# Performance work log

Hardware: AMD Instinct MI355X
Metric: run time of the kernel (lower is better)

The kernel has to match this reference:

```python
import jax, jax.numpy as jnp
import numpy as np

WS = 8      # window_size
SS = 4      # shift_size
DIM = 64
B, H, W = 4, 256, 256
EPS = 1e-12


def _conv(x, w, groups=1, pad=0):
    return jax.lax.conv_general_dilated(
        x, w, window_strides=(1, 1), padding=[(pad, pad), (pad, pad)],
        feature_group_count=groups,
        dimension_numbers=('NCHW', 'OIHW', 'NCHW'))


def _window_partition(x, ws):
    # Faithful to torch: permute (B,C,nh,ws,nw,ws)->(B,C,nh,nw,ws,ws) then flat view(-1,C,ws,ws)
    b, c, h, w = x.shape
    pb, pr = (-h) % ws, (-w) % ws
    if pb or pr:
        x = jnp.pad(x, ((0, 0), (0, 0), (0, pb), (0, pr)))
    h2, w2 = h + pb, w + pr
    x = x.reshape(b, c, h2 // ws, ws, w2 // ws, ws).transpose(0, 1, 2, 4, 3, 5)
    return x.reshape(-1, c, ws, ws)


def _window_reverse(win, ws, h, w):
    pb, pr = (-h) % ws, (-w) % ws
    h2, w2 = h + pb, w + pr
    b = win.shape[0] * ws * ws // (h2 * w2)
    x = win.reshape(b, -1, h2 // ws, w2 // ws, ws, ws).transpose(0, 1, 2, 4, 3, 5)
    x = x.reshape(b, -1, h2, w2)
    return x[:, :, :h, :w]


def _chan_attn(q, k, v, temp):
    # channel (transposed) attention on flattened window pixels
    n, c = q.shape[0], q.shape[1]
    q = q.reshape(n, c, -1)
    k = k.reshape(n, c, -1)
    v = v.reshape(n, c, -1)
    q = q / jnp.maximum(jnp.linalg.norm(q, axis=-1, keepdims=True), EPS)
    k = k / jnp.maximum(jnp.linalg.norm(k, axis=-1, keepdims=True), EPS)
    attn = jax.nn.softmax(jnp.einsum('ncd,nkd->nck', q, k) / temp, axis=-1)
    out = jnp.einsum('nck,nkd->ncd', attn, v)
    return out.reshape(n, c, WS, WS)


def setup_inputs() -> dict:
    key = jax.random.key(0)
    ks = jax.random.split(key, 10)
    C = DIM
    p = lambda k, s: jax.random.normal(k, s, jnp.float32) * 0.05
    return {
        'x': jax.random.normal(ks[0], (B, C, H, W), jnp.float32),
        'x_f': jax.random.normal(ks[1], (B, C, H, W), jnp.float32),
        'temperature': jnp.ones((1,), jnp.float32),
        'qk_w': p(ks[2], (2 * C, C, 1, 1)),
        'qk_dw_w': p(ks[3], (2 * C, 1, 3, 3)),
        'v_w': p(ks[4], (C, C, 1, 1)),
        'v_dw_w': p(ks[5], (C, 1, 3, 3)),
        'proj_w': p(ks[6], (C, C, 3, 3)),
        'proj1_w': p(ks[7], (C, C, 3, 3)),
        'qkv1_w': p(ks[8], (3 * C, C, 1, 1)),
        'qkv1_dw_w': p(ks[9], (3 * C, 1, 3, 3)),
    }


def reference(x, x_f, temperature, qk_w, qk_dw_w, v_w, v_dw_w,
              proj_w, proj1_w, qkv1_w, qkv1_dw_w):
    b, c, h, w = x.shape
    xw = _window_partition(x, WS)
    xfw = _window_partition(x_f, WS)

    qk = _conv(_conv(xfw, qk_w), qk_dw_w, groups=2 * c, pad=1)
    v = _conv(_conv(xw, v_w), v_dw_w, groups=c, pad=1)
    q, k = jnp.split(qk, 2, axis=1)
    out = _chan_attn(q, k, v, temperature)
    out = _conv(out, proj_w, pad=1)
    out = _window_reverse(out, WS, h, w)

    shift = jnp.roll(out, (-SS, -SS), axis=(2, 3))
    sw = _window_partition(shift, WS)
    qkv = _conv(_conv(sw, qkv1_w), qkv1_dw_w, groups=3 * c, pad=1)
    q, k, v = jnp.split(qkv, 3, axis=1)
    out = _chan_attn(q, k, v, temperature)
    out = _conv(out, proj1_w, pad=1)
    out = _window_reverse(out, WS, h, w)
    out = jnp.roll(out, (SS, SS), axis=(2, 3))
    return out
```

## Files before the change

### kernel.cpp

```cpp
#include <hip/hip_runtime.h>

typedef short v8s __attribute__((ext_vector_type(8)));
typedef _Float16 v8h __attribute__((ext_vector_type(8)));
typedef float v4f __attribute__((ext_vector_type(4)));
typedef unsigned short u16;

#define MFMA_F16(a, b, c) __builtin_amdgcn_mfma_f32_16x16x32_f16((a), (b), (c), 0, 0, 0)
#define XS 72

__device__ __forceinline__ u16 f16r(float x) {
    _Float16 h = (_Float16)x; u16 u; __builtin_memcpy(&u, &h, 2); return u;
}
__device__ __forceinline__ float f16f(u16 u) {
    _Float16 h; __builtin_memcpy(&h, &u, 2); return (float)h;
}

__device__ __forceinline__ void mm_frags(const u16* __restrict__ Ag,
                                         const u16* __restrict__ XB,
                                         int wv, int L, int q, v4f C[4])
{
#pragma unroll
    for (int nt = 0; nt < 4; ++nt) C[nt] = (v4f){0.f, 0.f, 0.f, 0.f};
#pragma unroll
    for (int kt = 0; kt < 2; ++kt) {
        v8h a = *(const v8h*)(Ag + (16 * wv + L) * 64 + kt * 32 + q * 8);
#pragma unroll
        for (int nt = 0; nt < 4; ++nt) {
            v8h b = *(const v8h*)(XB + (nt * 16 + L) * XS + kt * 32 + q * 8);
            C[nt] = MFMA_F16(a, b, C[nt]);
        }
    }
}
__device__ __forceinline__ void mm_store(const v4f C[4], u16* __restrict__ M,
                                         int wv, int L, int q)
{
    const int rowb = 16 * wv + 4 * q;
#pragma unroll
    for (int r = 0; r < 4; ++r)
#pragma unroll
        for (int nt = 0; nt < 4; ++nt)
            M[(rowb + r) * XS + nt * 16 + L] = f16r(C[nt][r]);
}
__device__ __forceinline__ void mm_stage(const u16* __restrict__ Ag,
                                         const u16* __restrict__ XB,
                                         u16* __restrict__ M,
                                         int wv, int L, int q)
{
    v4f C[4];
    mm_frags(Ag, XB, wv, L, q, C);
    mm_store(C, M, wv, L, q);
}

__device__ __forceinline__ void dw_read(const u16* __restrict__ M, int c, int r0,
                                        v8s raw[4])
{
#pragma unroll
    for (int r = 0; r < 4; ++r) {
        const int rr = r0 - 1 + r;
        raw[r] = ((unsigned)rr < 8u) ? *(const v8s*)(M + c * XS + rr * 8)
                                     : (v8s){0, 0, 0, 0, 0, 0, 0, 0};
    }
}

template <bool TR, bool NORM>
__device__ __forceinline__ void dw_write(const float* __restrict__ dwg,
                                         const v8s raw[4], int c, int r0,
                                         u16* __restrict__ Out)
{
    float w[9];
#pragma unroll
    for (int k = 0; k < 9; ++k) w[k] = dwg[c * 9 + k];
    float in[4][10];
#pragma unroll
    for (int r = 0; r < 4; ++r) {
        in[r][0] = 0.f; in[r][9] = 0.f;
#pragma unroll
        for (int j = 0; j < 8; ++j) in[r][j + 1] = f16f((u16)raw[r][j]);
    }
    float o[2][8];
#pragma unroll
    for (int rr = 0; rr < 2; ++rr)
#pragma unroll
        for (int j = 0; j < 8; ++j) {
            float s;
            s = w[0] * in[rr][j];
            s = fmaf(w[1], in[rr][j + 1], s);
            s = fmaf(w[2], in[rr][j + 2], s);
            s = fmaf(w[3], in[rr + 1][j], s);
            s = fmaf(w[4], in[rr + 1][j + 1], s);
            s = fmaf(w[5], in[rr + 1][j + 2], s);
            s = fmaf(w[6], in[rr + 2][j], s);
            s = fmaf(w[7], in[rr + 2][j + 1], s);
            s = fmaf(w[8], in[rr + 2][j + 2], s);
            o[rr][j] = s;
        }
    if (NORM) {
        float ss = 0.f;
#pragma unroll
        for (int rr = 0; rr < 2; ++rr)
#pragma unroll
            for (int j = 0; j < 8; ++j) ss = fmaf(o[rr][j], o[rr][j], ss);
        ss += __shfl_xor(ss, 1);
        ss += __shfl_xor(ss, 2);
        const float sc = 1.0f / fmaxf(sqrtf(ss), 1e-12f);
#pragma unroll
        for (int rr = 0; rr < 2; ++rr)
#pragma unroll
            for (int j = 0; j < 8; ++j) o[rr][j] *= sc;
    }
    if (TR) {
#pragma unroll
        for (int rr = 0; rr < 2; ++rr)
#pragma unroll
            for (int j = 0; j < 8; ++j)
                Out[((r0 + rr) * 8 + j) * XS + c] = f16r(o[rr][j]);
    } else {
#pragma unroll
        for (int rr = 0; rr < 2; ++rr) {
            v8s v;
#pragma unroll
            for (int j = 0; j < 8; ++j) v[j] = (short)f16r(o[rr][j]);
            *(v8s*)(Out + c * XS + (r0 + rr) * 8) = v;
        }
    }
}

__device__ __forceinline__ void mm_lds(const u16* __restrict__ Am,
                                       const u16* __restrict__ Bm,
                                       int wv, int L, int q, v4f C[4])
{
#pragma unroll
    for (int nt = 0; nt < 4; ++nt) C[nt] = (v4f){0.f, 0.f, 0.f, 0.f};
#pragma unroll
    for (int kt = 0; kt < 2; ++kt) {
        v8h a = *(const v8h*)(Am + (16 * wv + L) * XS + kt * 32 + q * 8);
#pragma unroll
        for (int nt = 0; nt < 4; ++nt) {
            v8h b = *(const v8h*)(Bm + (nt * 16 + L) * XS + kt * 32 + q * 8);
            C[nt] = MFMA_F16(a, b, C[nt]);
        }
    }
}

__device__ __forceinline__ void proj_mm(const u16* __restrict__ Wg,
                                        const u16* __restrict__ Ot,
                                        int wv, int L, int q, v4f C[4])
{
#pragma unroll
    for (int nt = 0; nt < 4; ++nt) C[nt] = (v4f){0.f, 0.f, 0.f, 0.f};
    const u16* arow = Wg + (16 * wv + L) * 576;
    const int pc = L & 7;
    const int prb = L >> 3;
#pragma unroll
    for (int tap = 0; tap < 9; ++tap) {
        const int dy = tap / 3 - 1, dx = tap % 3 - 1;
        const int spc = pc + dx;
        const bool vc = (unsigned)spc < 8u;
#pragma unroll
        for (int half = 0; half < 2; ++half) {
            v8h a = *(const v8h*)(arow + tap * 64 + half * 32 + q * 8);
#pragma unroll
            for (int nt = 0; nt < 4; ++nt) {
                const int spr = nt * 2 + prb + dy;
                v8h b = (v8h)0;
                if (vc && (unsigned)spr < 8u)
                    b = *(const v8h*)(Ot + (spr * 8 + spc) * XS + half * 32 + q * 8);
                C[nt] = MFMA_F16(a, b, C[nt]);
            }
        }
    }
}

__device__ __forceinline__ void softmax_to_lds(v4f S[4], float invt,
                                               u16* __restrict__ Am,
                                               int rowb, int L)
{
#pragma unroll
    for (int nt = 0; nt < 4; ++nt) S[nt] *= invt;
#pragma unroll
    for (int r = 0; r < 4; ++r) {
        float mx = fmaxf(fmaxf(S[0][r], S[1][r]), fmaxf(S[2][r], S[3][r]));
        mx = fmaxf(mx, __shfl_xor(mx, 1));
        mx = fmaxf(mx, __shfl_xor(mx, 2));
        mx = fmaxf(mx, __shfl_xor(mx, 4));
        mx = fmaxf(mx, __shfl_xor(mx, 8));
        float e0 = __expf(S[0][r] - mx);
        float e1 = __expf(S[1][r] - mx);
        float e2 = __expf(S[2][r] - mx);
        float e3 = __expf(S[3][r] - mx);
        float sm = e0 + e1 + e2 + e3;
        sm += __shfl_xor(sm, 1);
        sm += __shfl_xor(sm, 2);
        sm += __shfl_xor(sm, 4);
        sm += __shfl_xor(sm, 8);
        const float ri = 1.0f / sm;
        Am[(rowb + r) * XS + L +  0] = f16r(e0 * ri);
        Am[(rowb + r) * XS + L + 16] = f16r(e1 * ri);
        Am[(rowb + r) * XS + L + 32] = f16r(e2 * ri);
        Am[(rowb + r) * XS + L + 48] = f16r(e3 * ri);
    }
}

__global__ void prep(const float* __restrict__ qk_w, const float* __restrict__ v_w,
                     const float* __restrict__ qkv_w, const float* __restrict__ pw0,
                     const float* __restrict__ pw1, u16* __restrict__ Wb)
{
    int i = blockIdx.x * 256 + threadIdx.x;
    float v;
    if (i < 8192) v = qk_w[i];
    else if (i < 12288) v = v_w[i - 8192];
    else if (i < 24576) v = qkv_w[i - 12288];
    else {
        int j = i - 24576;
        const float* s = pw0;
        if (j >= 36864) { s = pw1; j -= 36864; }
        const int o = j / 576, kk = j % 576;
        const int tap = kk >> 6, c = kk & 63;
        v = s[o * 576 + c * 9 + tap];
    }
    Wb[i] = f16r(v);
}

__global__ __launch_bounds__(256, 4) void k1(
    const float* __restrict__ x, const float* __restrict__ xf,
    const float* __restrict__ temp_p,
    const float* __restrict__ qk_dw, const float* __restrict__ v_dw,
    const u16* __restrict__ Wqk, const u16* __restrict__ Wv,
    const u16* __restrict__ Wp0,
    u16* __restrict__ midb)
{
    __shared__ u16 B0[64 * XS], B1[64 * XS], B2[64 * XS], B3[64 * XS];
    const int t = threadIdx.x, n = blockIdx.x;
    const int lane = t & 63, wv = t >> 6, L = lane & 15, q = lane >> 4;
    const int rowb = 16 * wv + 4 * q;
    const size_t base = (size_t)n << 12;
    const float invt = 1.0f / temp_p[0];
    const int yp = t >> 4, xx0 = (t & 15) << 4;
    const int c2b = (yp >> 3) << 5, ir = (yp & 7) << 3;
    const int dc = t >> 2, dr0 = (t & 3) << 1;

    float4 rx[4];
    {
        const float* sf = xf + base + yp * 256 + xx0;
        const float* sx = x  + base + yp * 256 + xx0;
#pragma unroll
        for (int k = 0; k < 4; ++k) {
            float4 a = *(const float4*)(sf + 4 * k);
            rx[k] = *(const float4*)(sx + 4 * k);
            const int xx = xx0 + 4 * k;
            const int c = c2b + (xx >> 3), pb = ir + (xx & 7);
            B0[(pb + 0) * XS + c] = f16r(a.x);
            B0[(pb + 1) * XS + c] = f16r(a.y);
            B0[(pb + 2) * XS + c] = f16r(a.z);
            B0[(pb + 3) * XS + c] = f16r(a.w);
        }
    }
    __syncthreads();
    mm_stage(Wqk,        B0, B1, wv, L, q);
    mm_stage(Wqk + 4096, B0, B2, wv, L, q);
    __syncthreads();
    {
#pragma unroll
        for (int k = 0; k < 4; ++k) {
            const int xx = xx0 + 4 * k;
            const int c = c2b + (xx >> 3), pb = ir + (xx & 7);
            B3[(pb + 0) * XS + c] = f16r(rx[k].x);
            B3[(pb + 1) * XS + c] = f16r(rx[k].y);
            B3[(pb + 2) * XS + c] = f16r(rx[k].z);
            B3[(pb + 3) * XS + c] = f16r(rx[k].w);
        }
    }
    v8s rawA[4];
    dw_read(B1, dc, dr0, rawA);
    __syncthreads();
    mm_stage(Wv, B3, B0, wv, L, q);
    dw_write<false, true>(qk_dw, rawA, dc, dr0, B1);
    v8s rawB[4];
    dw_read(B2, dc, dr0, rawB);
    __syncthreads();
    dw_write<false, true>(qk_dw + 576, rawB, dc, dr0, B2);
    dw_read(B0, dc, dr0, rawA);
    dw_write<true, false>(v_dw, rawA, dc, dr0, B3);
    __syncthreads();
    v4f S[4];
    mm_lds(B1, B2, wv, L, q, S);
    softmax_to_lds(S, invt, B1, rowb, L);
    __syncthreads();
    v4f O[4];
    mm_lds(B1, B3, wv, L, q, O);
#pragma unroll
    for (int nt = 0; nt < 4; ++nt)
#pragma unroll
        for (int r = 0; r < 4; ++r)
            B2[(L + 16 * nt) * XS + rowb + r] = f16r(O[nt][r]);
    __syncthreads();
    v4f C[4];
    proj_mm(Wp0, B2, wv, L, q, C);
#pragma unroll
    for (int nt = 0; nt < 4; ++nt)
#pragma unroll
        for (int r = 0; r < 4; ++r) {
            const int o = rowb + r, p = L + 16 * nt;
            const int yy = ((o >> 5) << 3) + (p >> 3);
            const int xp = ((o & 31) << 3) + (p & 7);
            midb[base + yy * 256 + xp] = f16r(C[nt][r]);
        }
}

__global__ __launch_bounds__(256, 4) void k2(
    const u16* __restrict__ midb, const float* __restrict__ temp_p,
    const float* __restrict__ qkv_dw,
    const u16* __restrict__ Wqkv, const u16* __restrict__ Wp1,
    float* __restrict__ out)
{
    __shared__ u16 B0[64 * XS], B1[64 * XS], B2[64 * XS];
    const int t = threadIdx.x, m = blockIdx.x;
    const int lane = t & 63, wv = t >> 6, L = lane & 15, q = lane >> 4;
    const int rowb = 16 * wv + 4 * q;
    const int plane = m >> 4, mh2 = m & 15;
    const u16* img = midb + ((size_t)plane << 16);
    const float invt = 1.0f / temp_p[0];
    const int yp = t >> 4, xx0 = (t & 15) << 4;
    const int c2b = (yp >> 3) << 5, ir = (yp & 7) << 3;
    const int dc = t >> 2, dr0 = (t & 3) << 1;

    {
        const int row = (mh2 * 16 + 4 + yp) & 255;
#pragma unroll
        for (int k = 0; k < 4; ++k) {
            const int cc = (xx0 + 4 + 4 * k) & 255;
            ushort4 a = *(const ushort4*)(img + row * 256 + cc);
            const int xx = xx0 + 4 * k;
            const int c = c2b + (xx >> 3), pb = ir + (xx & 7);
            B0[(pb + 0) * XS + c] = a.x;
            B0[(pb + 1) * XS + c] = a.y;
            B0[(pb + 2) * XS + c] = a.z;
            B0[(pb + 3) * XS + c] = a.w;
        }
    }
    __syncthreads();
    mm_stage(Wqkv,        B0, B1, wv, L, q);
    mm_stage(Wqkv + 4096, B0, B2, wv, L, q);
    v4f VF[4];
    mm_frags(Wqkv + 8192, B0, wv, L, q, VF);
    __syncthreads();
    mm_store(VF, B0, wv, L, q);
    v8s rawQ[4];
    dw_read(B1, dc, dr0, rawQ);
    __syncthreads();
    dw_write<false, true>(qkv_dw, rawQ, dc, dr0, B1);
    v8s rawK[4];
    dw_read(B2, dc, dr0, rawK);
    v8s rawV[4];
    dw_read(B0, dc, dr0, rawV);
    __syncthreads();
    dw_write<false, true>(qkv_dw + 576, rawK, dc, dr0, B2);
    dw_write<true, false>(qkv_dw + 1152, rawV, dc, dr0, B0);
    __syncthreads();
    v4f S[4];
    mm_lds(B1, B2, wv, L, q, S);
    softmax_to_lds(S, invt, B1, rowb, L);
    v4f O[4];
    mm_lds(B1, B0, wv, L, q, O);
    __syncthreads();
#pragma unroll
    for (int nt = 0; nt < 4; ++nt)
#pragma unroll
        for (int r = 0; r < 4; ++r)
            B2[(L + 16 * nt) * XS + rowb + r] = f16r(O[nt][r]);
    __syncthreads();
    v4f C[4];
    proj_mm(Wp1, B2, wv, L, q, C);
    float* op = out + ((size_t)plane << 16);
#pragma unroll
    for (int nt = 0; nt < 4; ++nt)
#pragma unroll
        for (int r = 0; r < 4; ++r) {
            const int o = rowb + r, p = L + 16 * nt;
            const int R = mh2 * 16 + ((o >> 5) << 3) + (p >> 3);
            const int orow = (R + 4) & 255;
            const int ocol = ((o & 31) * 8 + (p & 7) + 4) & 255;
            op[orow * 256 + ocol] = C[nt][r];
        }
}

extern "C" void kernel_launch(void* const* d_in, const int* in_sizes, int n_in,
                              void* d_out, int out_size, void* d_ws, size_t ws_size,
                              hipStream_t stream)
{
    const float* x       = (const float*)d_in[0];
    const float* xf      = (const float*)d_in[1];
    const float* temp    = (const float*)d_in[2];
    const float* qk_w    = (const float*)d_in[3];
    const float* qk_dw   = (const float*)d_in[4];
    const float* v_w     = (const float*)d_in[5];
    const float* v_dw    = (const float*)d_in[6];
    const float* proj_w  = (const float*)d_in[7];
    const float* proj1_w = (const float*)d_in[8];
    const float* qkv1_w  = (const float*)d_in[9];
    const float* qkv1_dw = (const float*)d_in[10];
    float* out = (float*)d_out;

    u16* midb = (u16*)d_ws;
    u16* Wb   = (u16*)((char*)d_ws + 33554432);

    prep<<<384, 256, 0, stream>>>(qk_w, v_w, qkv1_w, proj_w, proj1_w, Wb);
    k1<<<4096, 256, 0, stream>>>(x, xf, temp, qk_dw, v_dw,
                                 Wb, Wb + 8192, Wb + 24576, midb);
    k2<<<4096, 256, 0, stream>>>(midb, temp, qkv1_dw,
                                 Wb + 12288, Wb + 61440, out);
}
```

Measured before the change: 291.8 us.

## Restructure k1 stage schedule to cut barriers and add MFMA wave priority

In k1, x and x_f are both converted into LDS in the initial load loop. The V projection is computed as register fragments alongside the QK projections, mirroring k2's schedule, which removes one barrier and a register-held staging of x. A barrier between softmax and the attention-V matmul is dropped. s_setprio raises wave priority around MFMA sections in both kernels so matrix work is favoured over other waves. These changes shift the buffer-role assignments, and dropping the barrier relies on each wave reading only the softmax rows it wrote.

```diff
diff --git a/kernel.cpp b/kernel.cpp
--- a/kernel.cpp
+++ b/kernel.cpp
@@ -239,55 +239,56 @@
     const int c2b = (yp >> 3) << 5, ir = (yp & 7) << 3;
     const int dc = t >> 2, dr0 = (t & 3) << 1;
 
-    float4 rx[4];
     {
         const float* sf = xf + base + yp * 256 + xx0;
         const float* sx = x  + base + yp * 256 + xx0;
 #pragma unroll
         for (int k = 0; k < 4; ++k) {
             float4 a = *(const float4*)(sf + 4 * k);
-            rx[k] = *(const float4*)(sx + 4 * k);
+            float4 b = *(const float4*)(sx + 4 * k);
             const int xx = xx0 + 4 * k;
             const int c = c2b + (xx >> 3), pb = ir + (xx & 7);
             B0[(pb + 0) * XS + c] = f16r(a.x);
             B0[(pb + 1) * XS + c] = f16r(a.y);
             B0[(pb + 2) * XS + c] = f16r(a.z);
             B0[(pb + 3) * XS + c] = f16r(a.w);
-        }
-    }
-    __syncthreads();
+            B3[(pb + 0) * XS + c] = f16r(b.x);
+            B3[(pb + 1) * XS + c] = f16r(b.y);
+            B3[(pb + 2) * XS + c] = f16r(b.z);
+            B3[(pb + 3) * XS + c] = f16r(b.w);
+        }
+    }
+    __syncthreads();
+    __builtin_amdgcn_s_setprio(1);
     mm_stage(Wqk,        B0, B1, wv, L, q);
     mm_stage(Wqk + 4096, B0, B2, wv, L, q);
-    __syncthreads();
-    {
-#pragma unroll
-        for (int k = 0; k < 4; ++k) {
-            const int xx = xx0 + 4 * k;
-            const int c = c2b + (xx >> 3), pb = ir + (xx & 7);
-            B3[(pb + 0) * XS + c] = f16r(rx[k].x);
-            B3[(pb + 1) * XS + c] = f16r(rx[k].y);
-            B3[(pb + 2) * XS + c] = f16r(rx[k].z);
-            B3[(pb + 3) * XS + c] = f16r(rx[k].w);
-        }
-    }
-    v8s rawA[4];
-    dw_read(B1, dc, dr0, rawA);
-    __syncthreads();
-    mm_stage(Wv, B3, B0, wv, L, q);
-    dw_write<false, true>(qk_dw, rawA, dc, dr0, B1);
-    v8s rawB[4];
-    dw_read(B2, dc, dr0, rawB);
-    __syncthreads();
-    dw_write<false, true>(qk_dw + 576, rawB, dc, dr0, B2);
-    dw_read(B0, dc, dr0, rawA);
-    dw_write<true, false>(v_dw, rawA, dc, dr0, B3);
+    v4f VF[4];
+    mm_frags(Wv, B3, wv, L, q, VF);
+    __builtin_amdgcn_s_setprio(0);
+    __syncthreads();
+    mm_store(VF, B3, wv, L, q);
+    v8s rawQ[4];
+    dw_read(B1, dc, dr0, rawQ);
+    __syncthreads();
+    dw_write<false, true>(qk_dw, rawQ, dc, dr0, B1);
+    v8s rawK[4];
+    dw_read(B2, dc, dr0, rawK);
+    v8s rawV[4];
+    dw_read(B3, dc, dr0, rawV);
+    __syncthreads();
+    dw_write<false, true>(qk_dw + 576, rawK, dc, dr0, B2);
+    dw_write<true, false>(v_dw, rawV, dc, dr0, B0);
     __syncthreads();
     v4f S[4];
+    __builtin_amdgcn_s_setprio(1);
     mm_lds(B1, B2, wv, L, q, S);
+    __builtin_amdgcn_s_setprio(0);
     softmax_to_lds(S, invt, B1, rowb, L);
-    __syncthreads();
     v4f O[4];
-    mm_lds(B1, B3, wv, L, q, O);
+    __builtin_amdgcn_s_setprio(1);
+    mm_lds(B1, B0, wv, L, q, O);
+    __builtin_amdgcn_s_setprio(0);
+    __syncthreads();
 #pragma unroll
     for (int nt = 0; nt < 4; ++nt)
 #pragma unroll
@@ -295,7 +296,9 @@
             B2[(L + 16 * nt) * XS + rowb + r] = f16r(O[nt][r]);
     __syncthreads();
     v4f C[4];
+    __builtin_amdgcn_s_setprio(1);
     proj_mm(Wp0, B2, wv, L, q, C);
+    __builtin_amdgcn_s_setprio(0);
 #pragma unroll
     for (int nt = 0; nt < 4; ++nt)
 #pragma unroll
@@ -339,10 +342,12 @@
         }
     }
     __syncthreads();
+    __builtin_amdgcn_s_setprio(1);
     mm_stage(Wqkv,        B0, B1, wv, L, q);
     mm_stage(Wqkv + 4096, B0, B2, wv, L, q);
     v4f VF[4];
     mm_frags(Wqkv + 8192, B0, wv, L, q, VF);
+    __builtin_amdgcn_s_setprio(0);
     __syncthreads();
     mm_store(VF, B0, wv, L, q);
     v8s rawQ[4];
@@ -358,10 +363,14 @@
     dw_write<true, false>(qkv_dw + 1152, rawV, dc, dr0, B0);
     __syncthreads();
     v4f S[4];
+    __builtin_amdgcn_s_setprio(1);
     mm_lds(B1, B2, wv, L, q, S);
+    __builtin_amdgcn_s_setprio(0);
     softmax_to_lds(S, invt, B1, rowb, L);
     v4f O[4];
+    __builtin_amdgcn_s_setprio(1);
     mm_lds(B1, B0, wv, L, q, O);
+    __builtin_amdgcn_s_setprio(0);
     __syncthreads();
 #pragma unroll
     for (int nt = 0; nt < 4; ++nt)
@@ -370,7 +379,9 @@
             B2[(L + 16 * nt) * XS + rowb + r] = f16r(O[nt][r]);
     __syncthreads();
     v4f C[4];
+    __builtin_amdgcn_s_setprio(1);
     proj_mm(Wp1, B2, wv, L, q, C);
+    __builtin_amdgcn_s_setprio(0);
     float* op = out + ((size_t)plane << 16);
 #pragma unroll
     for (int nt = 0; nt < 4; ++nt)
```

New measurement: 291.1 us. About the same (-0.2%).

## Process two window tiles per block in k1 and k2 to interleave work

Applied to the files above, without the earlier changes.

Each block in both kernels now handles two independent tiles, using doubled LDS buffers and interleaving their matmul, depthwise and softmax stages. This halves the block count and the barriers per tile, and gives the scheduler independent MFMA and LDS work to overlap. In exchange register and LDS use per block roughly doubles, and launch bounds drop to 2 blocks per SM, which lowers occupancy. k1's buffer usage is reorganised from four buffers to three per tile, with the V projection moved to register fragments.

```diff
diff --git a/kernel.cpp b/kernel.cpp
--- a/kernel.cpp
+++ b/kernel.cpp
@@ -221,7 +221,7 @@
     Wb[i] = f16r(v);
 }
 
-__global__ __launch_bounds__(256, 4) void k1(
+__global__ __launch_bounds__(256, 2) void k1(
     const float* __restrict__ x, const float* __restrict__ xf,
     const float* __restrict__ temp_p,
     const float* __restrict__ qk_dw, const float* __restrict__ v_dw,
@@ -229,73 +229,107 @@
     const u16* __restrict__ Wp0,
     u16* __restrict__ midb)
 {
-    __shared__ u16 B0[64 * XS], B1[64 * XS], B2[64 * XS], B3[64 * XS];
-    const int t = threadIdx.x, n = blockIdx.x;
+    __shared__ u16 B0a[64 * XS], B1a[64 * XS], B2a[64 * XS];
+    __shared__ u16 B0b[64 * XS], B1b[64 * XS], B2b[64 * XS];
+    const int t = threadIdx.x;
+    const int n0 = blockIdx.x << 1, n1 = n0 + 1;
     const int lane = t & 63, wv = t >> 6, L = lane & 15, q = lane >> 4;
     const int rowb = 16 * wv + 4 * q;
-    const size_t base = (size_t)n << 12;
+    const size_t base0 = (size_t)n0 << 12, base1 = (size_t)n1 << 12;
     const float invt = 1.0f / temp_p[0];
     const int yp = t >> 4, xx0 = (t & 15) << 4;
     const int c2b = (yp >> 3) << 5, ir = (yp & 7) << 3;
     const int dc = t >> 2, dr0 = (t & 3) << 1;
 
-    float4 rx[4];
+    float4 rx0[4], rx1[4];
     {
-        const float* sf = xf + base + yp * 256 + xx0;
-        const float* sx = x  + base + yp * 256 + xx0;
+        const float* sf0 = xf + base0 + yp * 256 + xx0;
+        const float* sx0 = x  + base0 + yp * 256 + xx0;
+        const float* sf1 = xf + base1 + yp * 256 + xx0;
+        const float* sx1 = x  + base1 + yp * 256 + xx0;
 #pragma unroll
         for (int k = 0; k < 4; ++k) {
-            float4 a = *(const float4*)(sf + 4 * k);
-            rx[k] = *(const float4*)(sx + 4 * k);
+            float4 a0 = *(const float4*)(sf0 + 4 * k);
+            float4 a1 = *(const float4*)(sf1 + 4 * k);
+            rx0[k] = *(const float4*)(sx0 + 4 * k);
+            rx1[k] = *(const float4*)(sx1 + 4 * k);
             const int xx = xx0 + 4 * k;
             const int c = c2b + (xx >> 3), pb = ir + (xx & 7);
-            B0[(pb + 0) * XS + c] = f16r(a.x);
-            B0[(pb + 1) * XS + c] = f16r(a.y);
-            B0[(pb + 2) * XS + c] = f16r(a.z);
-            B0[(pb + 3) * XS + c] = f16r(a.w);
-        }
-    }
-    __syncthreads();
-    mm_stage(Wqk,        B0, B1, wv, L, q);
-    mm_stage(Wqk + 4096, B0, B2, wv, L, q);
+            B0a[(pb + 0) * XS + c] = f16r(a0.x);
+            B0a[(pb + 1) * XS + c] = f16r(a0.y);
+            B0a[(pb + 2) * XS + c] = f16r(a0.z);
+            B0a[(pb + 3) * XS + c] = f16r(a0.w);
+            B0b[(pb + 0) * XS + c] = f16r(a1.x);
+            B0b[(pb + 1) * XS + c] = f16r(a1.y);
+            B0b[(pb + 2) * XS + c] = f16r(a1.z);
+            B0b[(pb + 3) * XS + c] = f16r(a1.w);
+        }
+    }
+    __syncthreads();
+    mm_stage(Wqk,        B0a, B1a, wv, L, q);
+    mm_stage(Wqk + 4096, B0a, B2a, wv, L, q);
+    mm_stage(Wqk,        B0b, B1b, wv, L, q);
+    mm_stage(Wqk + 4096, B0b, B2b, wv, L, q);
     __syncthreads();
     {
 #pragma unroll
         for (int k = 0; k < 4; ++k) {
             const int xx = xx0 + 4 * k;
             const int c = c2b + (xx >> 3), pb = ir + (xx & 7);
-            B3[(pb + 0) * XS + c] = f16r(rx[k].x);
-            B3[(pb + 1) * XS + c] = f16r(rx[k].y);
-            B3[(pb + 2) * XS + c] = f16r(rx[k].z);
-            B3[(pb + 3) * XS + c] = f16r(rx[k].w);
-        }
-    }
-    v8s rawA[4];
-    dw_read(B1, dc, dr0, rawA);
-    __syncthreads();
-    mm_stage(Wv, B3, B0, wv, L, q);
-    dw_write<false, true>(qk_dw, rawA, dc, dr0, B1);
-    v8s rawB[4];
-    dw_read(B2, dc, dr0, rawB);
-    __syncthreads();
-    dw_write<false, true>(qk_dw + 576, rawB, dc, dr0, B2);
-    dw_read(B0, dc, dr0, rawA);
-    dw_write<true, false>(v_dw, rawA, dc, dr0, B3);
-    __syncthreads();
-    v4f S[4];
-    mm_lds(B1, B2, wv, L, q, S);
-    softmax_to_lds(S, invt, B1, rowb, L);
-    __syncthreads();
-    v4f O[4];
-    mm_lds(B1, B3, wv, L, q, O);
+            B0a[(pb + 0) * XS + c] = f16r(rx0[k].x);
+            B0a[(pb + 1) * XS + c] = f16r(rx0[k].y);
+            B0a[(pb + 2) * XS + c] = f16r(rx0[k].z);
+            B0a[(pb + 3) * XS + c] = f16r(rx0[k].w);
+            B0b[(pb + 0) * XS + c] = f16r(rx1[k].x);
+            B0b[(pb + 1) * XS + c] = f16r(rx1[k].y);
+            B0b[(pb + 2) * XS + c] = f16r(rx1[k].z);
+            B0b[(pb + 3) * XS + c] = f16r(rx1[k].w);
+        }
+    }
+    v8s rawQ0[4], rawQ1[4];
+    dw_read(B1a, dc, dr0, rawQ0);
+    dw_read(B1b, dc, dr0, rawQ1);
+    __syncthreads();
+    v4f VF0[4], VF1[4];
+    mm_frags(Wv, B0a, wv, L, q, VF0);
+    mm_frags(Wv, B0b, wv, L, q, VF1);
+    dw_write<false, true>(qk_dw, rawQ0, dc, dr0, B1a);
+    dw_write<false, true>(qk_dw, rawQ1, dc, dr0, B1b);
+    v8s rawK0[4], rawK1[4];
+    dw_read(B2a, dc, dr0, rawK0);
+    dw_read(B2b, dc, dr0, rawK1);
+    __syncthreads();
+    mm_store(VF0, B0a, wv, L, q);
+    mm_store(VF1, B0b, wv, L, q);
+    dw_write<false, true>(qk_dw + 576, rawK0, dc, dr0, B2a);
+    dw_write<false, true>(qk_dw + 576, rawK1, dc, dr0, B2b);
+    __syncthreads();
+    v8s rawV0[4], rawV1[4];
+    dw_read(B0a, dc, dr0, rawV0);
+    dw_read(B0b, dc, dr0, rawV1);
+    v4f S0[4], S1[4];
+    mm_lds(B1a, B2a, wv, L, q, S0);
+    mm_lds(B1b, B2b, wv, L, q, S1);
+    softmax_to_lds(S0, invt, B1a, rowb, L);
+    softmax_to_lds(S1, invt, B1b, rowb, L);
+    __syncthreads();
+    dw_write<true, false>(v_dw, rawV0, dc, dr0, B0a);
+    dw_write<true, false>(v_dw, rawV1, dc, dr0, B0b);
+    __syncthreads();
+    v4f O0[4], O1[4];
+    mm_lds(B1a, B0a, wv, L, q, O0);
+    mm_lds(B1b, B0b, wv, L, q, O1);
 #pragma unroll
     for (int nt = 0; nt < 4; ++nt)
 #pragma unroll
-        for (int r = 0; r < 4; ++r)
-            B2[(L + 16 * nt) * XS + rowb + r] = f16r(O[nt][r]);
-    __syncthreads();
-    v4f C[4];
-    proj_mm(Wp0, B2, wv, L, q, C);
+        for (int r = 0; r < 4; ++r) {
+            B2a[(L + 16 * nt) * XS + rowb + r] = f16r(O0[nt][r]);
+            B2b[(L + 16 * nt) * XS + rowb + r] = f16r(O1[nt][r]);
+        }
+    __syncthreads();
+    v4f C0[4], C1[4];
+    proj_mm(Wp0, B2a, wv, L, q, C0);
+    proj_mm(Wp0, B2b, wv, L, q, C1);
 #pragma unroll
     for (int nt = 0; nt < 4; ++nt)
 #pragma unroll
@@ -303,84 +337,114 @@
             const int o = rowb + r, p = L + 16 * nt;
             const int yy = ((o >> 5) << 3) + (p >> 3);
             const int xp = ((o & 31) << 3) + (p & 7);
-            midb[base + yy * 256 + xp] = f16r(C[nt][r]);
-        }
-}
-
-__global__ __launch_bounds__(256, 4) void k2(
+            midb[base0 + yy * 256 + xp] = f16r(C0[nt][r]);
+            midb[base1 + yy * 256 + xp] = f16r(C1[nt][r]);
+        }
+}
+
+__global__ __launch_bounds__(256, 2) void k2(
     const u16* __restrict__ midb, const float* __restrict__ temp_p,
     const float* __restrict__ qkv_dw,
     const u16* __restrict__ Wqkv, const u16* __restrict__ Wp1,
     float* __restrict__ out)
 {
-    __shared__ u16 B0[64 * XS], B1[64 * XS], B2[64 * XS];
-    const int t = threadIdx.x, m = blockIdx.x;
+    __shared__ u16 B0a[64 * XS], B1a[64 * XS], B2a[64 * XS];
+    __shared__ u16 B0b[64 * XS], B1b[64 * XS], B2b[64 * XS];
+    const int t = threadIdx.x;
+    const int m0 = blockIdx.x << 1, m1 = m0 + 1;
     const int lane = t & 63, wv = t >> 6, L = lane & 15, q = lane >> 4;
     const int rowb = 16 * wv + 4 * q;
-    const int plane = m >> 4, mh2 = m & 15;
-    const u16* img = midb + ((size_t)plane << 16);
+    const int plane0 = m0 >> 4, mh0 = m0 & 15;
+    const int plane1 = m1 >> 4, mh1 = m1 & 15;
+    const u16* img0 = midb + ((size_t)plane0 << 16);
+    const u16* img1 = midb + ((size_t)plane1 << 16);
     const float invt = 1.0f / temp_p[0];
     const int yp = t >> 4, xx0 = (t & 15) << 4;
     const int c2b = (yp >> 3) << 5, ir = (yp & 7) << 3;
     const int dc = t >> 2, dr0 = (t & 3) << 1;
 
     {
-        const int row = (mh2 * 16 + 4 + yp) & 255;
+        const int row0 = (mh0 * 16 + 4 + yp) & 255;
+        const int row1 = (mh1 * 16 + 4 + yp) & 255;
 #pragma unroll
         for (int k = 0; k < 4; ++k) {
             const int cc = (xx0 + 4 + 4 * k) & 255;
-            ushort4 a = *(const ushort4*)(img + row * 256 + cc);
+            ushort4 a0 = *(const ushort4*)(img0 + row0 * 256 + cc);
+            ushort4 a1 = *(const ushort4*)(img1 + row1 * 256 + cc);
             const int xx = xx0 + 4 * k;
             const int c = c2b + (xx >> 3), pb = ir + (xx & 7);
-            B0[(pb + 0) * XS + c] = a.x;
-            B0[(pb + 1) * XS + c] = a.y;
-            B0[(pb + 2) * XS + c] = a.z;
-            B0[(pb + 3) * XS + c] = a.w;
-        }
-    }
-    __syncthreads();
-    mm_stage(Wqkv,        B0, B1, wv, L, q);
-    mm_stage(Wqkv + 4096, B0, B2, wv, L, q);
-    v4f VF[4];
-    mm_frags(Wqkv + 8192, B0, wv, L, q, VF);
-    __syncthreads();
-    mm_store(VF, B0, wv, L, q);
-    v8s rawQ[4];
-    dw_read(B1, dc, dr0, rawQ);
-    __syncthreads();
-    dw_write<false, true>(qkv_dw, rawQ, dc, dr0, B1);
-    v8s rawK[4];
-    dw_read(B2, dc, dr0, rawK);
-    v8s rawV[4];
-    dw_read(B0, dc, dr0, rawV);
-    __syncthreads();
-    dw_write<false, true>(qkv_dw + 576, rawK, dc, dr0, B2);
-    dw_write<true, false>(qkv_dw + 1152, rawV, dc, dr0, B0);
-    __syncthreads();
-    v4f S[4];
-    mm_lds(B1, B2, wv, L, q, S);
-    softmax_to_lds(S, invt, B1, rowb, L);
-    v4f O[4];
-    mm_lds(B1, B0, wv, L, q, O);
+            B0a[(pb + 0) * XS + c] = a0.x;
+            B0a[(pb + 1) * XS + c] = a0.y;
+            B0a[(pb + 2) * XS + c] = a0.z;
+            B0a[(pb + 3) * XS + c] = a0.w;
+            B0b[(pb + 0) * XS + c] = a1.x;
+            B0b[(pb + 1) * XS + c] = a1.y;
+            B0b[(pb + 2) * XS + c] = a1.z;
+            B0b[(pb + 3) * XS + c] = a1.w;
+        }
+    }
+    __syncthreads();
+    mm_stage(Wqkv,        B0a, B1a, wv, L, q);
+    mm_stage(Wqkv + 4096, B0a, B2a, wv, L, q);
+    v4f VF0[4], VF1[4];
+    mm_frags(Wqkv + 8192, B0a, wv, L, q, VF0);
+    mm_stage(Wqkv,        B0b, B1b, wv, L, q);
+    mm_stage(Wqkv + 4096, B0b, B2b, wv, L, q);
+    mm_frags(Wqkv + 8192, B0b, wv, L, q, VF1);
+    __syncthreads();
+    mm_store(VF0, B0a, wv, L, q);
+    mm_store(VF1, B0b, wv, L, q);
+    v8s rawQ0[4], rawQ1[4];
+    dw_read(B1a, dc, dr0, rawQ0);
+    dw_read(B1b, dc, dr0, rawQ1);
+    __syncthreads();
+    dw_write<false, true>(qkv_dw, rawQ0, dc, dr0, B1a);
+    dw_write<false, true>(qkv_dw, rawQ1, dc, dr0, B1b);
+    v8s rawK0[4], rawK1[4];
+    dw_read(B2a, dc, dr0, rawK0);
+    dw_read(B2b, dc, dr0, rawK1);
+    v8s rawV0[4], rawV1[4];
+    dw_read(B0a, dc, dr0, rawV0);
+    dw_read(B0b, dc, dr0, rawV1);
+    __syncthreads();
+    dw_write<false, true>(qkv_dw + 576, rawK0, dc, dr0, B2a);
+    dw_write<false, true>(qkv_dw + 576, rawK1, dc, dr0, B2b);
+    dw_write<true, false>(qkv_dw + 1152, rawV0, dc, dr0, B0a);
+    dw_write<true, false>(qkv_dw + 1152, rawV1, dc, dr0, B0b);
+    __syncthreads();
+    v4f S0[4], S1[4];
+    mm_lds(B1a, B2a, wv, L, q, S0);
+    mm_lds(B1b, B2b, wv, L, q, S1);
+    softmax_to_lds(S0, invt, B1a, rowb, L);
+    softmax_to_lds(S1, invt, B1b, rowb, L);
+    v4f O0[4], O1[4];
+    mm_lds(B1a, B0a, wv, L, q, O0);
+    mm_lds(B1b, B0b, wv, L, q, O1);
     __syncthreads();
 #pragma unroll
     for (int nt = 0; nt < 4; ++nt)
 #pragma unroll
-        for (int r = 0; r < 4; ++r)
-            B2[(L + 16 * nt) * XS + rowb + r] = f16r(O[nt][r]);
-    __syncthreads();
-    v4f C[4];
-    proj_mm(Wp1, B2, wv, L, q, C);
-    float* op = out + ((size_t)plane << 16);
+        for (int r = 0; r < 4; ++r) {
+            B2a[(L + 16 * nt) * XS + rowb + r] = f16r(O0[nt][r]);
+            B2b[(L + 16 * nt) * XS + rowb + r] = f16r(O1[nt][r]);
+        }
+    __syncthreads();
+    v4f C0[4], C1[4];
+    proj_mm(Wp1, B2a, wv, L, q, C0);
+    proj_mm(Wp1, B2b, wv, L, q, C1);
+    float* op0 = out + ((size_t)plane0 << 16);
+    float* op1 = out + ((size_t)plane1 << 16);
 #pragma unroll
     for (int nt = 0; nt < 4; ++nt)
 #pragma unroll
         for (int r = 0; r < 4; ++r) {
             const int o = rowb + r, p = L + 16 * nt;
-            const int R = mh2 * 16 + ((o >> 5) << 3) + (p >> 3);
-            const int orow = (R + 4) & 255;
+            const int yb = ((o >> 5) << 3) + (p >> 3);
             const int ocol = ((o & 31) * 8 + (p & 7) + 4) & 255;
-            op[orow * 256 + ocol] = C[nt][r];
+            const int orow0 = (mh0 * 16 + yb + 4) & 255;
+            const int orow1 = (mh1 * 16 + yb + 4) & 255;
+            op0[orow0 * 256 + ocol] = C0[nt][r];
+            op1[orow1 * 256 + ocol] = C1[nt][r];
         }
 }
 
@@ -405,8 +469,8 @@
     u16* Wb   = (u16*)((char*)d_ws + 33554432);
 
     prep<<<384, 256, 0, stream>>>(qk_w, v_w, qkv1_w, proj_w, proj1_w, Wb);
-    k1<<<4096, 256, 0, stream>>>(x, xf, temp, qk_dw, v_dw,
+    k1<<<2048, 256, 0, stream>>>(x, xf, temp, qk_dw, v_dw,
                                  Wb, Wb + 8192, Wb + 24576, midb);
-    k2<<<4096, 256, 0, stream>>>(midb, temp, qkv1_dw,
+    k2<<<2048, 256, 0, stream>>>(midb, temp, qkv1_dw,
                                  Wb + 12288, Wb + 61440, out);
 }
```

After: 322.3 us. +10.4%, slower.
